# Optimization experiments

Measured on AMD Instinct MI355X. Metric: run time of the kernel, lower is better.

The kernel has to match this reference:

```python
import jax, jax.numpy as jnp
import numpy as np

INFTY = 100000000.0


def setup_inputs() -> dict:
    key = jax.random.key(0)
    B, T, H = 512, 50, 128
    ks = jax.random.split(key, 11)
    s = 0.1
    return {
        "enc_outputs": jax.random.normal(ks[0], (B, T, H), jnp.float32),
        "h0": jax.random.normal(ks[1], (B, H), jnp.float32),
        "c0": jax.random.normal(ks[2], (B, H), jnp.float32),
        "W_ih": jax.random.normal(ks[3], (4 * H, H), jnp.float32) * s,
        "W_hh": jax.random.normal(ks[4], (4 * H, H), jnp.float32) * s,
        "b_ih": jax.random.normal(ks[5], (4 * H,), jnp.float32) * s,
        "b_hh": jax.random.normal(ks[6], (4 * H,), jnp.float32) * s,
        "go": jax.random.normal(ks[7], (1, H), jnp.float32) * s,
        "W_ref": jax.random.normal(ks[8], (H, H), jnp.float32) * s,
        "W_out": jax.random.normal(ks[9], (H, H), jnp.float32) * s,
        "v": jax.random.normal(ks[10], (H,), jnp.float32) * s,
    }


def _lstm_cell(x, h, c, W_ih, W_hh, b_ih, b_hh):
    # torch.nn.LSTMCell: gates ordered (i, f, g, o)
    gates = x @ W_ih.T + b_ih + h @ W_hh.T + b_hh  # [B, 4H]
    i, f, g, o = jnp.split(gates, 4, axis=-1)
    i = jax.nn.sigmoid(i)
    f = jax.nn.sigmoid(f)
    g = jnp.tanh(g)
    o = jax.nn.sigmoid(o)
    c_new = f * c + i * g
    return o * jnp.tanh(c_new), c_new


def reference(enc_outputs, h0, c0, W_ih, W_hh, b_ih, b_hh, go, W_ref, W_out, v):
    B, T, H = enc_outputs.shape
    # W_ref is linear and enc_outputs is fixed -> hoist out of the step loop
    enc_term = jnp.einsum('bth,oh->bto', enc_outputs, W_ref)  # [B, T, H]
    step_keys = jax.random.split(jax.random.key(42), T)

    def step(carry, k):
        h, c, mask, dec_input = carry
        h, c = _lstm_cell(dec_input, h, c, W_ih, W_hh, b_ih, b_hh)
        dec_term = (h @ W_out.T)[:, None, :]                              # [B, 1, H]
        scores = jnp.sum(v * jnp.tanh(enc_term + dec_term), axis=-1)     # [B, T]
        masked = scores - INFTY * mask                                   # kill visited
        loc = jax.random.categorical(k, masked)                          # [B] int
        logp = jnp.take_along_axis(jax.nn.log_softmax(masked, axis=-1),
                                   loc[:, None], axis=1)[:, 0]           # [B]
        mask = mask + jax.nn.one_hot(loc, T, dtype=mask.dtype)
        dec_input = jnp.take_along_axis(enc_outputs, loc[:, None, None], axis=1)[:, 0, :]
        return (h, c, mask, dec_input), (loc, logp)

    init = (h0, c0, jnp.zeros((B, T), enc_outputs.dtype),
            jnp.broadcast_to(go, (B, H)))
    _, (locs, logps) = jax.lax.scan(step, init, step_keys)  # locs: [T, B]
    tour = jnp.concatenate([locs.T, locs[0][:, None]], axis=1)  # [B, T+1] closed tour
    log_prob = jnp.sum(logps, axis=0)                           # [B]
    return log_prob, tour
```

## Files before the change

kernel.cpp:

```cpp
#include <hip/hip_runtime.h>
#include <stdint.h>

#define Bsz  512
#define Tlen 50
#define Hdim 128
#define GB   2
#define NBLK (Bsz/GB)
#define NTHR 1024
#define BIG  100000000.0f
#define TINYF 1.17549435e-38f

struct U2 { uint32_t a, b; };

__device__ __forceinline__ U2 tf2x32(uint32_t k0, uint32_t k1, uint32_t x0, uint32_t x1) {
  uint32_t k2 = k0 ^ k1 ^ 0x1BD11BDAu;
  x0 += k0; x1 += k1;
#define RR(r) { x0 += x1; x1 = (x1 << (r)) | (x1 >> (32 - (r))); x1 ^= x0; }
  RR(13) RR(15) RR(26) RR(6)
  x0 += k1; x1 += k2 + 1u;
  RR(17) RR(29) RR(16) RR(24)
  x0 += k2; x1 += k0 + 2u;
  RR(13) RR(15) RR(26) RR(6)
  x0 += k0; x1 += k1 + 3u;
  RR(17) RR(29) RR(16) RR(24)
  x0 += k1; x1 += k2 + 4u;
  RR(13) RR(15) RR(26) RR(6)
  x0 += k2; x1 += k0 + 5u;
#undef RR
  U2 r; r.a = x0; r.b = x1; return r;
}

__device__ __forceinline__ float fast_tanh(float x) {
  float xc = fminf(fmaxf(x, -9.0f), 9.0f);
  float e = __expf(2.0f * xc);
  return (e - 1.0f) / (e + 1.0f);
}

__global__ void prep_kernel(const float* __restrict__ W_ih, const float* __restrict__ W_hh,
                            const float* __restrict__ W_out, const float* __restrict__ W_ref,
                            float* __restrict__ WTP, float* __restrict__ WoT4,
                            float* __restrict__ WrT4) {
  int idx = blockIdx.x * blockDim.x + threadIdx.x;
  if (idx < 131072) {
    int j  = idx & 3;
    int r  = (idx >> 2) & 511;
    int kb = idx >> 11;
    int k  = kb * 4 + j;
    WTP[idx] = (k < Hdim) ? W_ih[r * Hdim + k] : W_hh[r * Hdim + (k - Hdim)];
  } else if (idx < 131072 + 16384) {
    int i2 = idx - 131072;
    int j = i2 & 3, o = (i2 >> 2) & 127, kb = i2 >> 9;
    WoT4[i2] = W_out[o * Hdim + (kb * 4 + j)];
  } else if (idx < 131072 + 32768) {
    int i3 = idx - 147456;
    int j = i3 & 3, o = (i3 >> 2) & 127, hb = i3 >> 9;
    WrT4[i3] = W_ref[o * Hdim + (hb * 4 + j)];
  }
}

__global__ __launch_bounds__(NTHR) void actor_main(
    const float* __restrict__ enc, const float* __restrict__ h0,
    const float* __restrict__ c0, const float* __restrict__ b_ih,
    const float* __restrict__ b_hh, const float* __restrict__ go,
    const float* __restrict__ v, const float* __restrict__ WTP,
    const float* __restrict__ WoT4, const float* __restrict__ WrT4,
    float* __restrict__ out)
{
  __shared__ __align__(16) float s_encterm[GB][Tlen][Hdim];
  __shared__ __align__(16) float s_xh[GB][2 * Hdim];
  __shared__ __align__(16) float s_c[GB][Hdim];
  __shared__ __align__(16) float s_gates[GB][4 * Hdim];
  __shared__ __align__(16) float s_ax[GB][4 * Hdim];
  __shared__ __align__(16) float s_ah[GB][4 * Hdim];
  __shared__ __align__(16) float s_dec[GB][Hdim];
  __shared__ float s_scores[GB][Tlen];
  __shared__ float s_mask[GB][Tlen];
  __shared__ __align__(16) float s_bih[4 * Hdim];
  __shared__ __align__(16) float s_bhh[4 * Hdim];
  __shared__ __align__(16) float s_v[Hdim];
  __shared__ float s_logp[GB];

  const int tid = threadIdx.x;
  const int b0  = blockIdx.x * GB;

  for (int i = tid; i < 4 * Hdim; i += NTHR) { s_bih[i] = b_ih[i]; s_bhh[i] = b_hh[i]; }
  for (int i = tid; i < Hdim; i += NTHR) s_v[i] = v[i];
  for (int i = tid; i < GB * Hdim; i += NTHR) {
    int b = i >> 7, jj = i & 127;
    s_xh[b][jj]        = go[jj];
    s_xh[b][Hdim + jj] = h0[(size_t)(b0 + b) * Hdim + jj];
    s_c[b][jj]         = c0[(size_t)(b0 + b) * Hdim + jj];
  }
  for (int i = tid; i < GB * Tlen; i += NTHR) (&s_mask[0][0])[i] = 0.0f;
  if (tid < GB) s_logp[tid] = 0.0f;

  {
    const float4* Wr4 = (const float4*)WrT4;
    for (int oidx = tid; oidx < GB * Tlen * Hdim; oidx += NTHR) {
      int b = oidx / (Tlen * Hdim);
      int rem = oidx - b * (Tlen * Hdim);
      int t = rem >> 7, o = rem & 127;
      const float4* ep4 = (const float4*)(enc + ((size_t)(b0 + b) * Tlen + t) * Hdim);
      float acc = 0.0f;
#pragma unroll 4
      for (int hb = 0; hb < 32; ++hb) {
        float4 e4 = ep4[hb];
        float4 w4 = Wr4[hb * 128 + o];
        acc = fmaf(e4.x, w4.x, acc); acc = fmaf(e4.y, w4.y, acc);
        acc = fmaf(e4.z, w4.z, acc); acc = fmaf(e4.w, w4.w, acc);
      }
      s_encterm[b][t][o] = acc;
    }
  }
  __syncthreads();

  const float4* W4  = (const float4*)WTP;
  const float4* Wo4 = (const float4*)WoT4;

  for (int t = 0; t < Tlen; ++t) {
    {
      int r    = tid & 511;
      int part = tid >> 9;
      int xoff = part * Hdim;
      int woff = part * 32;
      const float4* vA = (const float4*)&s_xh[0][xoff];
      const float4* vB = (const float4*)&s_xh[1][xoff];
      float a0 = 0.f, a1 = 0.f;
#pragma unroll 4
      for (int kb = 0; kb < 32; ++kb) {
        float4 w4 = W4[(kb + woff) * 512 + r];
        float4 f0 = vA[kb];
        float4 f1 = vB[kb];
        a0 = fmaf(f0.x, w4.x, a0); a0 = fmaf(f0.y, w4.y, a0);
        a0 = fmaf(f0.z, w4.z, a0); a0 = fmaf(f0.w, w4.w, a0);
        a1 = fmaf(f1.x, w4.x, a1); a1 = fmaf(f1.y, w4.y, a1);
        a1 = fmaf(f1.z, w4.z, a1); a1 = fmaf(f1.w, w4.w, a1);
      }
      if (part == 0) { s_ax[0][r] = a0; s_ax[1][r] = a1; }
      else           { s_ah[0][r] = a0; s_ah[1][r] = a1; }
    }
    __syncthreads();

    {
      int r = tid & 511, b = tid >> 9;
      s_gates[b][r] = ((s_ax[b][r] + s_bih[r]) + s_ah[b][r]) + s_bhh[r];
    }
    __syncthreads();

    if (tid < GB * Hdim) {
      int b = tid >> 7, jj = tid & 127;
      float gi = s_gates[b][jj];
      float gf = s_gates[b][Hdim + jj];
      float gg = s_gates[b][2 * Hdim + jj];
      float gob = s_gates[b][3 * Hdim + jj];
      float i_ = 1.0f / (1.0f + expf(-gi));
      float f_ = 1.0f / (1.0f + expf(-gf));
      float g_ = tanhf(gg);
      float o_ = 1.0f / (1.0f + expf(-gob));
      float cn = f_ * s_c[b][jj] + i_ * g_;
      s_c[b][jj] = cn;
      s_xh[b][Hdim + jj] = o_ * tanhf(cn);
    }
    __syncthreads();

    if (tid < GB * Hdim) {
      int b = tid >> 7, o = tid & 127;
      float acc = 0.0f;
#pragma unroll 4
      for (int kb = 0; kb < 32; ++kb) {
        float4 w4 = Wo4[kb * 128 + o];
        float4 h4 = *(const float4*)&s_xh[b][Hdim + kb * 4];
        acc = fmaf(h4.x, w4.x, acc); acc = fmaf(h4.y, w4.y, acc);
        acc = fmaf(h4.z, w4.z, acc); acc = fmaf(h4.w, w4.w, acc);
      }
      s_dec[b][o] = acc;
    }
    __syncthreads();

    {
      int w = tid >> 6, lane = tid & 63;
      float vlo = s_v[lane], vhi = s_v[lane + 64];
      for (int task = w; task < GB * Tlen; task += (NTHR / 64)) {
        int b = task / Tlen, tt = task - b * Tlen;
        float p0 = s_encterm[b][tt][lane]      + s_dec[b][lane];
        float p1 = s_encterm[b][tt][lane + 64] + s_dec[b][lane + 64];
        float val = vlo * fast_tanh(p0) + vhi * fast_tanh(p1);
        for (int off = 32; off; off >>= 1) val += __shfl_down(val, off);
        if (lane == 0) s_scores[b][tt] = val;
      }
    }
    __syncthreads();

    {
      int w = tid >> 6;
      if (w < GB) {
        int b = w, lane = tid & 63;
        int bg = b0 + b;
        U2 sk = tf2x32(0u, 42u, 0u, (uint32_t)t);
        float masked_v = -3.0e38f, val = -3.0e38f;
        if (lane < Tlen) {
          float sc = s_scores[b][lane];
          float mk = s_mask[b][lane];
          masked_v = sc - BIG * mk;
          U2 rb = tf2x32(sk.a, sk.b, 0u, (uint32_t)(bg * Tlen + lane));
          uint32_t bits = rb.a ^ rb.b;
          float f = __uint_as_float((bits >> 9) | 0x3f800000u) - 1.0f;
          float u = fmaxf(f, TINYF);
          float gum = -logf(-logf(u));
          val = masked_v + gum;
        }
        float bv = val; int bi = (tid & 63);
        for (int off = 32; off; off >>= 1) {
          float ov = __shfl_down(bv, off);
          int   oi = __shfl_down(bi, off);
          if (ov > bv || (ov == bv && oi < bi)) { bv = ov; bi = oi; }
        }
        bi = __shfl(bi, 0);
        float mx = masked_v;
        for (int off = 32; off; off >>= 1) mx = fmaxf(mx, __shfl_down(mx, off));
        mx = __shfl(mx, 0);
        float ex = (lane < Tlen) ? expf(masked_v - mx) : 0.0f;
        for (int off = 32; off; off >>= 1) ex += __shfl_down(ex, off);
        ex = __shfl(ex, 0);
        float msel = __shfl(masked_v, bi);
        float logp = (msel - mx) - logf(ex);
        if (lane == 0) {
          s_logp[b] += logp;
          s_mask[b][bi] += 1.0f;
          out[Bsz + (size_t)bg * (Tlen + 1) + t] = (float)bi;
          if (t == 0) out[Bsz + (size_t)bg * (Tlen + 1) + Tlen] = (float)bi;
        }
        const float* ep = enc + ((size_t)bg * Tlen + bi) * Hdim;
        s_xh[b][lane]      = ep[lane];
        s_xh[b][lane + 64] = ep[lane + 64];
      }
    }
    __syncthreads();
  }

  if (tid < GB) out[b0 + tid] = s_logp[tid];
}

extern "C" void kernel_launch(void* const* d_in, const int* in_sizes, int n_in,
                              void* d_out, int out_size, void* d_ws, size_t ws_size,
                              hipStream_t stream) {
  const float* enc   = (const float*)d_in[0];
  const float* h0    = (const float*)d_in[1];
  const float* c0    = (const float*)d_in[2];
  const float* W_ih  = (const float*)d_in[3];
  const float* W_hh  = (const float*)d_in[4];
  const float* b_ih  = (const float*)d_in[5];
  const float* b_hh  = (const float*)d_in[6];
  const float* go    = (const float*)d_in[7];
  const float* W_ref = (const float*)d_in[8];
  const float* W_out = (const float*)d_in[9];
  const float* v     = (const float*)d_in[10];
  float* out = (float*)d_out;

  float* WTP  = (float*)d_ws;
  float* WoT4 = WTP + 131072;
  float* WrT4 = WoT4 + 16384;

  prep_kernel<<<640, 256, 0, stream>>>(W_ih, W_hh, W_out, W_ref, WTP, WoT4, WrT4);
  actor_main<<<NBLK, NTHR, 0, stream>>>(enc, h0, c0, b_ih, b_hh, go, v,
                                        WTP, WoT4, WrT4, out);
}
```

Measured before the change: 636.2 us.

## Overlap recurrent W_hh matvec with decoder and scoring phases, cache W_out in LDS

```diff
diff --git a/kernel.cpp b/kernel.cpp
--- a/kernel.cpp
+++ b/kernel.cpp
@@ -69,10 +69,10 @@
   __shared__ __align__(16) float s_encterm[GB][Tlen][Hdim];
   __shared__ __align__(16) float s_xh[GB][2 * Hdim];
   __shared__ __align__(16) float s_c[GB][Hdim];
-  __shared__ __align__(16) float s_gates[GB][4 * Hdim];
   __shared__ __align__(16) float s_ax[GB][4 * Hdim];
   __shared__ __align__(16) float s_ah[GB][4 * Hdim];
   __shared__ __align__(16) float s_dec[GB][Hdim];
+  __shared__ __align__(16) float4 s_wout4[32 * 128];
   __shared__ float s_scores[GB][Tlen];
   __shared__ float s_mask[GB][Tlen];
   __shared__ __align__(16) float s_bih[4 * Hdim];
@@ -93,6 +93,10 @@
   }
   for (int i = tid; i < GB * Tlen; i += NTHR) (&s_mask[0][0])[i] = 0.0f;
   if (tid < GB) s_logp[tid] = 0.0f;
+  {
+    const float4* src = (const float4*)WoT4;
+    for (int i = tid; i < 32 * 128; i += NTHR) s_wout4[i] = src[i];
+  }
 
   {
     const float4* Wr4 = (const float4*)WrT4;
@@ -114,45 +118,42 @@
   }
   __syncthreads();
 
-  const float4* W4  = (const float4*)WTP;
-  const float4* Wo4 = (const float4*)WoT4;
+  const float4* W4 = (const float4*)WTP;
+
+  {
+    int r    = tid & 511;
+    int part = tid >> 9;
+    int xoff = part * Hdim;
+    int woff = part * 32;
+    const float4* vA = (const float4*)&s_xh[0][xoff];
+    const float4* vB = (const float4*)&s_xh[1][xoff];
+    float a0 = 0.f, a1 = 0.f;
+#pragma unroll 8
+    for (int kb = 0; kb < 32; ++kb) {
+      float4 w4 = W4[(kb + woff) * 512 + r];
+      float4 f0 = vA[kb];
+      float4 f1 = vB[kb];
+      a0 = fmaf(f0.x, w4.x, a0); a0 = fmaf(f0.y, w4.y, a0);
+      a0 = fmaf(f0.z, w4.z, a0); a0 = fmaf(f0.w, w4.w, a0);
+      a1 = fmaf(f1.x, w4.x, a1); a1 = fmaf(f1.y, w4.y, a1);
+      a1 = fmaf(f1.z, w4.z, a1); a1 = fmaf(f1.w, w4.w, a1);
+    }
+    if (part == 0) { s_ax[0][r] = a0; s_ax[1][r] = a1; }
+    else           { s_ah[0][r] = a0; s_ah[1][r] = a1; }
+  }
+  __syncthreads();
 
   for (int t = 0; t < Tlen; ++t) {
-    {
-      int r    = tid & 511;
-      int part = tid >> 9;
-      int xoff = part * Hdim;
-      int woff = part * 32;
-      const float4* vA = (const float4*)&s_xh[0][xoff];
-      const float4* vB = (const float4*)&s_xh[1][xoff];
-      float a0 = 0.f, a1 = 0.f;
-#pragma unroll 4
-      for (int kb = 0; kb < 32; ++kb) {
-        float4 w4 = W4[(kb + woff) * 512 + r];
-        float4 f0 = vA[kb];
-        float4 f1 = vB[kb];
-        a0 = fmaf(f0.x, w4.x, a0); a0 = fmaf(f0.y, w4.y, a0);
-        a0 = fmaf(f0.z, w4.z, a0); a0 = fmaf(f0.w, w4.w, a0);
-        a1 = fmaf(f1.x, w4.x, a1); a1 = fmaf(f1.y, w4.y, a1);
-        a1 = fmaf(f1.z, w4.z, a1); a1 = fmaf(f1.w, w4.w, a1);
-      }
-      if (part == 0) { s_ax[0][r] = a0; s_ax[1][r] = a1; }
-      else           { s_ah[0][r] = a0; s_ah[1][r] = a1; }
-    }
-    __syncthreads();
-
-    {
-      int r = tid & 511, b = tid >> 9;
-      s_gates[b][r] = ((s_ax[b][r] + s_bih[r]) + s_ah[b][r]) + s_bhh[r];
-    }
-    __syncthreads();
+    const bool not_last = (t < Tlen - 1);
+    float ahA = 0.f, ahB = 0.f;
+    const int r = tid & 511;
 
     if (tid < GB * Hdim) {
       int b = tid >> 7, jj = tid & 127;
-      float gi = s_gates[b][jj];
-      float gf = s_gates[b][Hdim + jj];
-      float gg = s_gates[b][2 * Hdim + jj];
-      float gob = s_gates[b][3 * Hdim + jj];
+      float gi  = ((s_ax[b][jj]            + s_bih[jj])            + s_ah[b][jj])            + s_bhh[jj];
+      float gf  = ((s_ax[b][Hdim + jj]     + s_bih[Hdim + jj])     + s_ah[b][Hdim + jj])     + s_bhh[Hdim + jj];
+      float gg  = ((s_ax[b][2*Hdim + jj]   + s_bih[2*Hdim + jj])   + s_ah[b][2*Hdim + jj])   + s_bhh[2*Hdim + jj];
+      float gob = ((s_ax[b][3*Hdim + jj]   + s_bih[3*Hdim + jj])   + s_ah[b][3*Hdim + jj])   + s_bhh[3*Hdim + jj];
       float i_ = 1.0f / (1.0f + expf(-gi));
       float f_ = 1.0f / (1.0f + expf(-gf));
       float g_ = tanhf(gg);
@@ -168,19 +169,32 @@
       float acc = 0.0f;
 #pragma unroll 4
       for (int kb = 0; kb < 32; ++kb) {
-        float4 w4 = Wo4[kb * 128 + o];
+        float4 w4 = s_wout4[kb * 128 + o];
         float4 h4 = *(const float4*)&s_xh[b][Hdim + kb * 4];
         acc = fmaf(h4.x, w4.x, acc); acc = fmaf(h4.y, w4.y, acc);
         acc = fmaf(h4.z, w4.z, acc); acc = fmaf(h4.w, w4.w, acc);
       }
       s_dec[b][o] = acc;
-    }
-    __syncthreads();
-
-    {
+    } else if (tid >= 512 && not_last) {
+      const float4* vA = (const float4*)&s_xh[0][Hdim];
+      const float4* vB = (const float4*)&s_xh[1][Hdim];
+#pragma unroll 8
+      for (int kb = 0; kb < 16; ++kb) {
+        float4 w4 = W4[(kb + 32) * 512 + r];
+        float4 f0 = vA[kb];
+        float4 f1 = vB[kb];
+        ahA = fmaf(f0.x, w4.x, ahA); ahA = fmaf(f0.y, w4.y, ahA);
+        ahA = fmaf(f0.z, w4.z, ahA); ahA = fmaf(f0.w, w4.w, ahA);
+        ahB = fmaf(f1.x, w4.x, ahB); ahB = fmaf(f1.y, w4.y, ahB);
+        ahB = fmaf(f1.z, w4.z, ahB); ahB = fmaf(f1.w, w4.w, ahB);
+      }
+    }
+    __syncthreads();
+
+    if (tid < 512) {
       int w = tid >> 6, lane = tid & 63;
       float vlo = s_v[lane], vhi = s_v[lane + 64];
-      for (int task = w; task < GB * Tlen; task += (NTHR / 64)) {
+      for (int task = w; task < GB * Tlen; task += 8) {
         int b = task / Tlen, tt = task - b * Tlen;
         float p0 = s_encterm[b][tt][lane]      + s_dec[b][lane];
         float p1 = s_encterm[b][tt][lane + 64] + s_dec[b][lane + 64];
@@ -188,6 +202,20 @@
         for (int off = 32; off; off >>= 1) val += __shfl_down(val, off);
         if (lane == 0) s_scores[b][tt] = val;
       }
+    } else if (not_last) {
+      const float4* vA = (const float4*)&s_xh[0][Hdim];
+      const float4* vB = (const float4*)&s_xh[1][Hdim];
+#pragma unroll 8
+      for (int kb = 16; kb < 32; ++kb) {
+        float4 w4 = W4[(kb + 32) * 512 + r];
+        float4 f0 = vA[kb];
+        float4 f1 = vB[kb];
+        ahA = fmaf(f0.x, w4.x, ahA); ahA = fmaf(f0.y, w4.y, ahA);
+        ahA = fmaf(f0.z, w4.z, ahA); ahA = fmaf(f0.w, w4.w, ahA);
+        ahB = fmaf(f1.x, w4.x, ahB); ahB = fmaf(f1.y, w4.y, ahB);
+        ahB = fmaf(f1.z, w4.z, ahB); ahB = fmaf(f1.w, w4.w, ahB);
+      }
+      s_ah[0][r] = ahA; s_ah[1][r] = ahB;
     }
     __syncthreads();
 
@@ -236,6 +264,24 @@
       }
     }
     __syncthreads();
+
+    if (tid < 512 && not_last) {
+      const float4* vA = (const float4*)&s_xh[0][0];
+      const float4* vB = (const float4*)&s_xh[1][0];
+      float a0 = 0.f, a1 = 0.f;
+#pragma unroll 8
+      for (int kb = 0; kb < 32; ++kb) {
+        float4 w4 = W4[kb * 512 + r];
+        float4 f0 = vA[kb];
+        float4 f1 = vB[kb];
+        a0 = fmaf(f0.x, w4.x, a0); a0 = fmaf(f0.y, w4.y, a0);
+        a0 = fmaf(f0.z, w4.z, a0); a0 = fmaf(f0.w, w4.w, a0);
+        a1 = fmaf(f1.x, w4.x, a1); a1 = fmaf(f1.y, w4.y, a1);
+        a1 = fmaf(f1.z, w4.z, a1); a1 = fmaf(f1.w, w4.w, a1);
+      }
+      s_ax[0][r] = a0; s_ax[1][r] = a1;
+    }
+    __syncthreads();
   }
 
   if (tid < GB) out[b0 + tid] = s_logp[tid];
```

After: 775.2 us. 21.8% more time.

## Use one batch row per block and overlap the h-projection with attention scoring

Applied to the files above, without the earlier changes.

```diff
diff --git a/kernel.cpp b/kernel.cpp
--- a/kernel.cpp
+++ b/kernel.cpp
@@ -4,8 +4,7 @@
 #define Bsz  512
 #define Tlen 50
 #define Hdim 128
-#define GB   2
-#define NBLK (Bsz/GB)
+#define NBLK Bsz
 #define NTHR 1024
 #define BIG  100000000.0f
 #define TINYF 1.17549435e-38f
@@ -58,7 +57,7 @@
   }
 }
 
-__global__ __launch_bounds__(NTHR) void actor_main(
+__global__ __launch_bounds__(NTHR, 8) void actor_main(
     const float* __restrict__ enc, const float* __restrict__ h0,
     const float* __restrict__ c0, const float* __restrict__ b_ih,
     const float* __restrict__ b_hh, const float* __restrict__ go,
@@ -66,41 +65,37 @@
     const float* __restrict__ WoT4, const float* __restrict__ WrT4,
     float* __restrict__ out)
 {
-  __shared__ __align__(16) float s_encterm[GB][Tlen][Hdim];
-  __shared__ __align__(16) float s_xh[GB][2 * Hdim];
-  __shared__ __align__(16) float s_c[GB][Hdim];
-  __shared__ __align__(16) float s_gates[GB][4 * Hdim];
-  __shared__ __align__(16) float s_ax[GB][4 * Hdim];
-  __shared__ __align__(16) float s_ah[GB][4 * Hdim];
-  __shared__ __align__(16) float s_dec[GB][Hdim];
-  __shared__ float s_scores[GB][Tlen];
-  __shared__ float s_mask[GB][Tlen];
+  __shared__ __align__(16) float s_encterm[Tlen][Hdim];
+  __shared__ __align__(16) float s_xh[2 * Hdim];
+  __shared__ __align__(16) float s_c[Hdim];
+  __shared__ __align__(16) float s_ax[4 * Hdim];
+  __shared__ __align__(16) float s_ah[4 * Hdim];
+  __shared__ __align__(16) float s_dec[Hdim];
+  __shared__ float s_scores[Tlen];
+  __shared__ float s_mask[Tlen];
   __shared__ __align__(16) float s_bih[4 * Hdim];
   __shared__ __align__(16) float s_bhh[4 * Hdim];
   __shared__ __align__(16) float s_v[Hdim];
-  __shared__ float s_logp[GB];
+  __shared__ float s_logp;
 
   const int tid = threadIdx.x;
-  const int b0  = blockIdx.x * GB;
+  const int bg  = blockIdx.x;
 
   for (int i = tid; i < 4 * Hdim; i += NTHR) { s_bih[i] = b_ih[i]; s_bhh[i] = b_hh[i]; }
   for (int i = tid; i < Hdim; i += NTHR) s_v[i] = v[i];
-  for (int i = tid; i < GB * Hdim; i += NTHR) {
-    int b = i >> 7, jj = i & 127;
-    s_xh[b][jj]        = go[jj];
-    s_xh[b][Hdim + jj] = h0[(size_t)(b0 + b) * Hdim + jj];
-    s_c[b][jj]         = c0[(size_t)(b0 + b) * Hdim + jj];
-  }
-  for (int i = tid; i < GB * Tlen; i += NTHR) (&s_mask[0][0])[i] = 0.0f;
-  if (tid < GB) s_logp[tid] = 0.0f;
+  if (tid < Hdim) {
+    s_xh[tid]        = go[tid];
+    s_xh[Hdim + tid] = h0[(size_t)bg * Hdim + tid];
+    s_c[tid]         = c0[(size_t)bg * Hdim + tid];
+  }
+  for (int i = tid; i < Tlen; i += NTHR) s_mask[i] = 0.0f;
+  if (tid == 0) s_logp = 0.0f;
 
   {
     const float4* Wr4 = (const float4*)WrT4;
-    for (int oidx = tid; oidx < GB * Tlen * Hdim; oidx += NTHR) {
-      int b = oidx / (Tlen * Hdim);
-      int rem = oidx - b * (Tlen * Hdim);
-      int t = rem >> 7, o = rem & 127;
-      const float4* ep4 = (const float4*)(enc + ((size_t)(b0 + b) * Tlen + t) * Hdim);
+    for (int oidx = tid; oidx < Tlen * Hdim; oidx += NTHR) {
+      int t = oidx >> 7, o = oidx & 127;
+      const float4* ep4 = (const float4*)(enc + ((size_t)bg * Tlen + t) * Hdim);
       float acc = 0.0f;
 #pragma unroll 4
       for (int hb = 0; hb < 32; ++hb) {
@@ -109,7 +104,7 @@
         acc = fmaf(e4.x, w4.x, acc); acc = fmaf(e4.y, w4.y, acc);
         acc = fmaf(e4.z, w4.z, acc); acc = fmaf(e4.w, w4.w, acc);
       }
-      s_encterm[b][t][o] = acc;
+      s_encterm[t][o] = acc;
     }
   }
   __syncthreads();
@@ -117,128 +112,148 @@
   const float4* W4  = (const float4*)WTP;
   const float4* Wo4 = (const float4*)WoT4;
 
+  {
+    int r    = tid & 511;
+    int part = tid >> 9;
+    const float4* vA = (const float4*)&s_xh[part * Hdim];
+    int woff = part * 32;
+    float a0 = 0.f;
+#pragma unroll 4
+    for (int kb = 0; kb < 32; ++kb) {
+      float4 w4 = W4[(kb + woff) * 512 + r];
+      float4 f0 = vA[kb];
+      a0 = fmaf(f0.x, w4.x, a0); a0 = fmaf(f0.y, w4.y, a0);
+      a0 = fmaf(f0.z, w4.z, a0); a0 = fmaf(f0.w, w4.w, a0);
+    }
+    if (part == 0) s_ax[r] = a0; else s_ah[r] = a0;
+  }
+  __syncthreads();
+
   for (int t = 0; t < Tlen; ++t) {
-    {
-      int r    = tid & 511;
-      int part = tid >> 9;
-      int xoff = part * Hdim;
-      int woff = part * 32;
-      const float4* vA = (const float4*)&s_xh[0][xoff];
-      const float4* vB = (const float4*)&s_xh[1][xoff];
-      float a0 = 0.f, a1 = 0.f;
-#pragma unroll 4
-      for (int kb = 0; kb < 32; ++kb) {
-        float4 w4 = W4[(kb + woff) * 512 + r];
-        float4 f0 = vA[kb];
-        float4 f1 = vB[kb];
-        a0 = fmaf(f0.x, w4.x, a0); a0 = fmaf(f0.y, w4.y, a0);
-        a0 = fmaf(f0.z, w4.z, a0); a0 = fmaf(f0.w, w4.w, a0);
-        a1 = fmaf(f1.x, w4.x, a1); a1 = fmaf(f1.y, w4.y, a1);
-        a1 = fmaf(f1.z, w4.z, a1); a1 = fmaf(f1.w, w4.w, a1);
-      }
-      if (part == 0) { s_ax[0][r] = a0; s_ax[1][r] = a1; }
-      else           { s_ah[0][r] = a0; s_ah[1][r] = a1; }
-    }
-    __syncthreads();
-
-    {
-      int r = tid & 511, b = tid >> 9;
-      s_gates[b][r] = ((s_ax[b][r] + s_bih[r]) + s_ah[b][r]) + s_bhh[r];
-    }
-    __syncthreads();
-
-    if (tid < GB * Hdim) {
-      int b = tid >> 7, jj = tid & 127;
-      float gi = s_gates[b][jj];
-      float gf = s_gates[b][Hdim + jj];
-      float gg = s_gates[b][2 * Hdim + jj];
-      float gob = s_gates[b][3 * Hdim + jj];
+    const bool not_last = (t < Tlen - 1);
+    float ahA = 0.f;
+    const int r = tid & 511;
+
+    if (tid < Hdim) {
+      int jj = tid;
+      float gi  = ((s_ax[jj]          + s_bih[jj])          + s_ah[jj])          + s_bhh[jj];
+      float gf  = ((s_ax[Hdim + jj]   + s_bih[Hdim + jj])   + s_ah[Hdim + jj])   + s_bhh[Hdim + jj];
+      float gg  = ((s_ax[2*Hdim + jj] + s_bih[2*Hdim + jj]) + s_ah[2*Hdim + jj]) + s_bhh[2*Hdim + jj];
+      float gob = ((s_ax[3*Hdim + jj] + s_bih[3*Hdim + jj]) + s_ah[3*Hdim + jj]) + s_bhh[3*Hdim + jj];
       float i_ = 1.0f / (1.0f + expf(-gi));
       float f_ = 1.0f / (1.0f + expf(-gf));
       float g_ = tanhf(gg);
       float o_ = 1.0f / (1.0f + expf(-gob));
-      float cn = f_ * s_c[b][jj] + i_ * g_;
-      s_c[b][jj] = cn;
-      s_xh[b][Hdim + jj] = o_ * tanhf(cn);
-    }
-    __syncthreads();
-
-    if (tid < GB * Hdim) {
-      int b = tid >> 7, o = tid & 127;
+      float cn = f_ * s_c[jj] + i_ * g_;
+      s_c[jj] = cn;
+      s_xh[Hdim + jj] = o_ * tanhf(cn);
+    }
+    __syncthreads();
+
+    if (tid < Hdim) {
+      int o = tid;
       float acc = 0.0f;
 #pragma unroll 4
       for (int kb = 0; kb < 32; ++kb) {
         float4 w4 = Wo4[kb * 128 + o];
-        float4 h4 = *(const float4*)&s_xh[b][Hdim + kb * 4];
+        float4 h4 = *(const float4*)&s_xh[Hdim + kb * 4];
         acc = fmaf(h4.x, w4.x, acc); acc = fmaf(h4.y, w4.y, acc);
         acc = fmaf(h4.z, w4.z, acc); acc = fmaf(h4.w, w4.w, acc);
       }
-      s_dec[b][o] = acc;
-    }
-    __syncthreads();
-
-    {
+      s_dec[o] = acc;
+    } else if (tid >= 512 && not_last) {
+      const float4* vH = (const float4*)&s_xh[Hdim];
+#pragma unroll 4
+      for (int kb = 0; kb < 16; ++kb) {
+        float4 w4 = W4[(kb + 32) * 512 + r];
+        float4 f0 = vH[kb];
+        ahA = fmaf(f0.x, w4.x, ahA); ahA = fmaf(f0.y, w4.y, ahA);
+        ahA = fmaf(f0.z, w4.z, ahA); ahA = fmaf(f0.w, w4.w, ahA);
+      }
+    }
+    __syncthreads();
+
+    if (tid < 512) {
       int w = tid >> 6, lane = tid & 63;
       float vlo = s_v[lane], vhi = s_v[lane + 64];
-      for (int task = w; task < GB * Tlen; task += (NTHR / 64)) {
-        int b = task / Tlen, tt = task - b * Tlen;
-        float p0 = s_encterm[b][tt][lane]      + s_dec[b][lane];
-        float p1 = s_encterm[b][tt][lane + 64] + s_dec[b][lane + 64];
+      for (int task = w; task < Tlen; task += 8) {
+        float p0 = s_encterm[task][lane]      + s_dec[lane];
+        float p1 = s_encterm[task][lane + 64] + s_dec[lane + 64];
         float val = vlo * fast_tanh(p0) + vhi * fast_tanh(p1);
         for (int off = 32; off; off >>= 1) val += __shfl_down(val, off);
-        if (lane == 0) s_scores[b][tt] = val;
-      }
-    }
-    __syncthreads();
-
-    {
-      int w = tid >> 6;
-      if (w < GB) {
-        int b = w, lane = tid & 63;
-        int bg = b0 + b;
-        U2 sk = tf2x32(0u, 42u, 0u, (uint32_t)t);
-        float masked_v = -3.0e38f, val = -3.0e38f;
-        if (lane < Tlen) {
-          float sc = s_scores[b][lane];
-          float mk = s_mask[b][lane];
-          masked_v = sc - BIG * mk;
-          U2 rb = tf2x32(sk.a, sk.b, 0u, (uint32_t)(bg * Tlen + lane));
-          uint32_t bits = rb.a ^ rb.b;
-          float f = __uint_as_float((bits >> 9) | 0x3f800000u) - 1.0f;
-          float u = fmaxf(f, TINYF);
-          float gum = -logf(-logf(u));
-          val = masked_v + gum;
-        }
-        float bv = val; int bi = (tid & 63);
-        for (int off = 32; off; off >>= 1) {
-          float ov = __shfl_down(bv, off);
-          int   oi = __shfl_down(bi, off);
-          if (ov > bv || (ov == bv && oi < bi)) { bv = ov; bi = oi; }
-        }
-        bi = __shfl(bi, 0);
-        float mx = masked_v;
-        for (int off = 32; off; off >>= 1) mx = fmaxf(mx, __shfl_down(mx, off));
-        mx = __shfl(mx, 0);
-        float ex = (lane < Tlen) ? expf(masked_v - mx) : 0.0f;
-        for (int off = 32; off; off >>= 1) ex += __shfl_down(ex, off);
-        ex = __shfl(ex, 0);
-        float msel = __shfl(masked_v, bi);
-        float logp = (msel - mx) - logf(ex);
-        if (lane == 0) {
-          s_logp[b] += logp;
-          s_mask[b][bi] += 1.0f;
-          out[Bsz + (size_t)bg * (Tlen + 1) + t] = (float)bi;
-          if (t == 0) out[Bsz + (size_t)bg * (Tlen + 1) + Tlen] = (float)bi;
-        }
-        const float* ep = enc + ((size_t)bg * Tlen + bi) * Hdim;
-        s_xh[b][lane]      = ep[lane];
-        s_xh[b][lane + 64] = ep[lane + 64];
-      }
-    }
-    __syncthreads();
-  }
-
-  if (tid < GB) out[b0 + tid] = s_logp[tid];
+        if (lane == 0) s_scores[task] = val;
+      }
+    } else if (not_last) {
+      const float4* vH = (const float4*)&s_xh[Hdim];
+#pragma unroll 4
+      for (int kb = 16; kb < 32; ++kb) {
+        float4 w4 = W4[(kb + 32) * 512 + r];
+        float4 f0 = vH[kb];
+        ahA = fmaf(f0.x, w4.x, ahA); ahA = fmaf(f0.y, w4.y, ahA);
+        ahA = fmaf(f0.z, w4.z, ahA); ahA = fmaf(f0.w, w4.w, ahA);
+      }
+      s_ah[r] = ahA;
+    }
+    __syncthreads();
+
+    if (tid < 64) {
+      int lane = tid;
+      U2 sk = tf2x32(0u, 42u, 0u, (uint32_t)t);
+      float masked_v = -3.0e38f, val = -3.0e38f;
+      if (lane < Tlen) {
+        float sc = s_scores[lane];
+        float mk = s_mask[lane];
+        masked_v = sc - BIG * mk;
+        U2 rb = tf2x32(sk.a, sk.b, 0u, (uint32_t)(bg * Tlen + lane));
+        uint32_t bits = rb.a ^ rb.b;
+        float f = __uint_as_float((bits >> 9) | 0x3f800000u) - 1.0f;
+        float u = fmaxf(f, TINYF);
+        float gum = -logf(-logf(u));
+        val = masked_v + gum;
+      }
+      float bv = val; int bi = lane;
+      for (int off = 32; off; off >>= 1) {
+        float ov = __shfl_down(bv, off);
+        int   oi = __shfl_down(bi, off);
+        if (ov > bv || (ov == bv && oi < bi)) { bv = ov; bi = oi; }
+      }
+      bi = __shfl(bi, 0);
+      float mx = masked_v;
+      for (int off = 32; off; off >>= 1) mx = fmaxf(mx, __shfl_down(mx, off));
+      mx = __shfl(mx, 0);
+      float ex = (lane < Tlen) ? expf(masked_v - mx) : 0.0f;
+      for (int off = 32; off; off >>= 1) ex += __shfl_down(ex, off);
+      ex = __shfl(ex, 0);
+      float msel = __shfl(masked_v, bi);
+      float logp = (msel - mx) - logf(ex);
+      if (lane == 0) {
+        s_logp += logp;
+        s_mask[bi] += 1.0f;
+        out[Bsz + (size_t)bg * (Tlen + 1) + t] = (float)bi;
+        if (t == 0) out[Bsz + (size_t)bg * (Tlen + 1) + Tlen] = (float)bi;
+      }
+      const float* ep = enc + ((size_t)bg * Tlen + bi) * Hdim;
+      s_xh[lane]      = ep[lane];
+      s_xh[lane + 64] = ep[lane + 64];
+    }
+    __syncthreads();
+
+    if (tid < 512 && not_last) {
+      const float4* vX = (const float4*)&s_xh[0];
+      float a0 = 0.f;
+#pragma unroll 4
+      for (int kb = 0; kb < 32; ++kb) {
+        float4 w4 = W4[kb * 512 + r];
+        float4 f0 = vX[kb];
+        a0 = fmaf(f0.x, w4.x, a0); a0 = fmaf(f0.y, w4.y, a0);
+        a0 = fmaf(f0.z, w4.z, a0); a0 = fmaf(f0.w, w4.w, a0);
+      }
+      s_ax[r] = a0;
+    }
+    __syncthreads();
+  }
+
+  if (tid == 0) out[bg] = s_logp;
 }
 
 extern "C" void kernel_launch(void* const* d_in, const int* in_sizes, int n_in,
```

After: 754.1 us. 18.5% more time.
